# Kernel optimization log

Hardware: AMD Instinct MI355X
Metric: run time of the kernel (lower is better)

## Reference

```python
import jax, jax.numpy as jnp
import numpy as np

H = 512; W = 512; PH = 16; PW = 16; Q = 3; JITTER = 1e-06
NH = H // PH; NW = W // PW; P = NH * NW
B = 64


def setup_inputs() -> dict:
    key = jax.random.key(0)
    k0, k1, k2, k3, k4 = jax.random.split(key, 5)
    x = jax.random.normal(k0, (B, H, W), dtype=jnp.float32)
    logits = jax.random.normal(k1, (P, Q), dtype=jnp.float32)
    mu = jax.random.normal(k2, (P, Q, 2), dtype=jnp.float32) * 0.3
    sigma = jnp.exp(jax.random.normal(k3, (P, Q, 2), dtype=jnp.float32) * 0.3)
    bias = jax.random.normal(k4, (P, PH, PW), dtype=jnp.float32)
    return {"x": x, "logits": logits, "mu": mu, "sigma": sigma, "bias": bias}


def _make_S(logits, mu, sigma):
    # logits: (P,Q), mu/sigma: (P,Q,2) -> S: (P,PH,PW)
    w = jax.nn.softmax(logits, axis=-1)            # (P,Q)
    fy = jnp.fft.fftfreq(PH).astype(jnp.float32)   # (PH,)
    fx = jnp.fft.fftfreq(PW).astype(jnp.float32)   # (PW,)
    mu_y = mu[..., 0][:, :, None, None]            # (P,Q,1,1)
    mu_x = mu[..., 1][:, :, None, None]
    sg_y = sigma[..., 0][:, :, None, None]
    sg_x = sigma[..., 1][:, :, None, None]
    fy_b = fy[None, None, :, None]                 # (1,1,PH,1)
    fx_b = fx[None, None, None, :]                 # (1,1,1,PW)
    g1 = jnp.exp(-0.5 * (((fy_b - mu_y) / sg_y) ** 2 + ((fx_b - mu_x) / sg_x) ** 2))
    g2 = jnp.exp(-0.5 * (((fy_b + mu_y) / sg_y) ** 2 + ((fx_b + mu_x) / sg_x) ** 2))
    # weighted sum over mixture components Q
    S = jnp.einsum('pq,pqhw->phw', w, g1 + g2) + JITTER
    return S


def reference(x, logits, mu, sigma, bias):
    # x: (B,H,W) -> (B,H,W)
    S = _make_S(logits, mu, sigma)                                  # (P,PH,PW)
    x_p = x.reshape(B, NH, PH, NW, PW)
    x_p = x_p.transpose(1, 3, 0, 2, 4).reshape(P, B, PH, PW)        # (P,B,PH,PW)
    Xf = jnp.fft.fftn(x_p, axes=(-2, -1))                           # complex64
    y_p = jnp.fft.ifftn(Xf * S[:, None, :, :], axes=(-2, -1)).real  # (P,B,PH,PW)
    y_p = y_p + bias[:, None, :, :]
    y = y_p.reshape(NH, NW, B, PH, PW)
    y = y.transpose(2, 0, 3, 1, 4).reshape(B, H, W)
    return y
```

## Files before the change

kernel.cpp:

```cpp
#include <hip/hip_runtime.h>
#include <math.h>

#define HH 512
#define WW 512
#define PHH 16
#define PWW 16
#define QQ 3
#define NHH 32
#define NWW 32
#define PP 1024
#define BB 64

__device__ __constant__ float TWC[8] = {
    1.0f,  0.92387953251f,  0.70710678119f,  0.38268343236f,
    0.0f, -0.38268343236f, -0.70710678119f, -0.92387953251f};
__device__ __constant__ float TWS[8] = {
    0.0f, -0.38268343236f, -0.70710678119f, -0.92387953251f,
   -1.0f, -0.92387953251f, -0.70710678119f, -0.38268343236f};

template <int SGN>
__device__ __forceinline__ void fft16(float* re, float* im) {
#define SWAP_(a, b)                              \
  { float t = re[a]; re[a] = re[b]; re[b] = t;   \
    t = im[a]; im[a] = im[b]; im[b] = t; }
  SWAP_(1, 8) SWAP_(2, 4) SWAP_(3, 12) SWAP_(5, 10) SWAP_(7, 14) SWAP_(11, 13)
#undef SWAP_
#pragma unroll
  for (int len = 2; len <= 16; len <<= 1) {
    const int half = len >> 1;
    const int tstep = 16 / len;
#pragma unroll
    for (int i = 0; i < 16; i += len) {
#pragma unroll
      for (int j = 0; j < half; ++j) {
        const float wr = TWC[j * tstep];
        const float wi = (SGN > 0) ? TWS[j * tstep] : -TWS[j * tstep];
        const int a = i + j;
        const int c = i + j + half;
        const float tr = re[c] * wr - im[c] * wi;
        const float ti = re[c] * wi + im[c] * wr;
        re[c] = re[a] - tr;
        im[c] = im[a] - ti;
        re[a] = re[a] + tr;
        im[a] = im[a] + ti;
      }
    }
  }
}

__global__ __launch_bounds__(256) void psm_kernel(
    const float* __restrict__ x, const float* __restrict__ logits,
    const float* __restrict__ mu, const float* __restrict__ sigma,
    const float* __restrict__ bias, float* __restrict__ out) {
  __shared__ float S_lds[256];
  __shared__ float t_re[16 * 272];
  __shared__ float t_im[16 * 272];

  const int tid = threadIdx.x;
  const int p = blockIdx.x >> 2;
  const int b0 = (blockIdx.x & 3) << 4;
  const int g = tid >> 4;
  const int r = tid & 15;
  const int b = b0 + g;
  const int nh = p >> 5;
  const int nw = p & 31;

  {
    const int fy_i = tid >> 4;
    const int fx_i = tid & 15;
    const float fy = (float)(fy_i < 8 ? fy_i : fy_i - 16) * (1.0f / 16.0f);
    const float fx = (float)(fx_i < 8 ? fx_i : fx_i - 16) * (1.0f / 16.0f);
    const float l0 = logits[p * QQ + 0];
    const float l1 = logits[p * QQ + 1];
    const float l2 = logits[p * QQ + 2];
    const float lm = fmaxf(l0, fmaxf(l1, l2));
    const float e0 = __expf(l0 - lm);
    const float e1 = __expf(l1 - lm);
    const float e2 = __expf(l2 - lm);
    const float inv = 1.0f / (e0 + e1 + e2);
    const float wq[3] = {e0 * inv, e1 * inv, e2 * inv};
    float s = 0.0f;
#pragma unroll
    for (int q = 0; q < QQ; ++q) {
      const float muy = mu[(p * QQ + q) * 2 + 0];
      const float mux = mu[(p * QQ + q) * 2 + 1];
      const float isy = 1.0f / sigma[(p * QQ + q) * 2 + 0];
      const float isx = 1.0f / sigma[(p * QQ + q) * 2 + 1];
      const float dy1 = (fy - muy) * isy;
      const float dx1 = (fx - mux) * isx;
      const float dy2 = (fy + muy) * isy;
      const float dx2 = (fx + mux) * isx;
      const float g1 = __expf(-0.5f * (dy1 * dy1 + dx1 * dx1));
      const float g2 = __expf(-0.5f * (dy2 * dy2 + dx2 * dx2));
      s += wq[q] * (g1 + g2);
    }
    S_lds[tid] = (s + 1e-6f) * (1.0f / 256.0f);
  }
  __syncthreads();

  const size_t rowoff =
      (size_t)b * (HH * WW) + (size_t)(nh * PHH + r) * WW + (size_t)(nw * PWW);
  const float* xrow = x + rowoff;
  float re[16], im[16];
#pragma unroll
  for (int c4 = 0; c4 < 4; ++c4) {
    const float4 v = ((const float4*)xrow)[c4];
    re[c4 * 4 + 0] = v.x;
    re[c4 * 4 + 1] = v.y;
    re[c4 * 4 + 2] = v.z;
    re[c4 * 4 + 3] = v.w;
  }
#pragma unroll
  for (int c = 0; c < 16; ++c) im[c] = 0.0f;

  fft16<1>(re, im);

  float* mre = &t_re[g * 272];
  float* mim = &t_im[g * 272];
#pragma unroll
  for (int c = 0; c < 16; ++c) {
    mre[r * 17 + c] = re[c];
    mim[r * 17 + c] = im[c];
  }
  __syncthreads();
#pragma unroll
  for (int k = 0; k < 16; ++k) {
    re[k] = mre[k * 17 + r];
    im[k] = mim[k * 17 + r];
  }
  __syncthreads();

  fft16<1>(re, im);
#pragma unroll
  for (int k = 0; k < 16; ++k) {
    const float s = S_lds[k * 16 + r];
    re[k] *= s;
    im[k] *= s;
  }
  fft16<-1>(re, im);

#pragma unroll
  for (int k = 0; k < 16; ++k) {
    mre[k * 17 + r] = re[k];
    mim[k * 17 + r] = im[k];
  }
  __syncthreads();
#pragma unroll
  for (int c = 0; c < 16; ++c) {
    re[c] = mre[r * 17 + c];
    im[c] = mim[r * 17 + c];
  }

  fft16<-1>(re, im);

  const float* brow = bias + (size_t)p * 256 + (size_t)r * 16;
  float* orow = out + rowoff;
#pragma unroll
  for (int c4 = 0; c4 < 4; ++c4) {
    const float4 bv = ((const float4*)brow)[c4];
    float4 o;
    o.x = re[c4 * 4 + 0] + bv.x;
    o.y = re[c4 * 4 + 1] + bv.y;
    o.z = re[c4 * 4 + 2] + bv.z;
    o.w = re[c4 * 4 + 3] + bv.w;
    ((float4*)orow)[c4] = o;
  }
}

extern "C" void kernel_launch(void* const* d_in, const int* in_sizes, int n_in,
                              void* d_out, int out_size, void* d_ws,
                              size_t ws_size, hipStream_t stream) {
  (void)in_sizes;
  (void)n_in;
  (void)out_size;
  (void)d_ws;
  (void)ws_size;
  const float* x = (const float*)d_in[0];
  const float* logits = (const float*)d_in[1];
  const float* mu = (const float*)d_in[2];
  const float* sigma = (const float*)d_in[3];
  const float* bias = (const float*)d_in[4];
  float* out = (float*)d_out;

  psm_kernel<<<dim3(PP * 4), dim3(256), 0, stream>>>(x, logits, mu, sigma,
                                                     bias, out);
}
```

Before: 148.0 us.

## Replace LDS transposes with wavefront shuffle transposes and prefetch input rows

```diff
diff --git a/kernel.cpp b/kernel.cpp
--- a/kernel.cpp
+++ b/kernel.cpp
@@ -48,13 +48,35 @@
   }
 }
 
+__device__ __forceinline__ void transpose16(float* re, float* im, int r) {
+#pragma unroll
+  for (int s = 1; s <= 8; s <<= 1) {
+    const bool hi = (r & s) != 0;
+#pragma unroll
+    for (int j0 = 0; j0 < 16; ++j0) {
+      if ((j0 & s) == 0) {
+        const int j1 = j0 | s;
+        float sr = hi ? re[j0] : re[j1];
+        float si = hi ? im[j0] : im[j1];
+        sr = __shfl_xor(sr, s, 64);
+        si = __shfl_xor(si, s, 64);
+        if (hi) {
+          re[j0] = sr;
+          im[j0] = si;
+        } else {
+          re[j1] = sr;
+          im[j1] = si;
+        }
+      }
+    }
+  }
+}
+
 __global__ __launch_bounds__(256) void psm_kernel(
     const float* __restrict__ x, const float* __restrict__ logits,
     const float* __restrict__ mu, const float* __restrict__ sigma,
     const float* __restrict__ bias, float* __restrict__ out) {
   __shared__ float S_lds[256];
-  __shared__ float t_re[16 * 272];
-  __shared__ float t_im[16 * 272];
 
   const int tid = threadIdx.x;
   const int p = blockIdx.x >> 2;
@@ -64,6 +86,14 @@
   const int b = b0 + g;
   const int nh = p >> 5;
   const int nw = p & 31;
+
+  const size_t rowoff =
+      (size_t)b * (HH * WW) + (size_t)(nh * PHH + r) * WW + (size_t)(nw * PWW);
+  const float* xrow = x + rowoff;
+  float4 xv0 = ((const float4*)xrow)[0];
+  float4 xv1 = ((const float4*)xrow)[1];
+  float4 xv2 = ((const float4*)xrow)[2];
+  float4 xv3 = ((const float4*)xrow)[3];
 
   {
     const int fy_i = tid >> 4;
@@ -98,38 +128,16 @@
   }
   __syncthreads();
 
-  const size_t rowoff =
-      (size_t)b * (HH * WW) + (size_t)(nh * PHH + r) * WW + (size_t)(nw * PWW);
-  const float* xrow = x + rowoff;
   float re[16], im[16];
-#pragma unroll
-  for (int c4 = 0; c4 < 4; ++c4) {
-    const float4 v = ((const float4*)xrow)[c4];
-    re[c4 * 4 + 0] = v.x;
-    re[c4 * 4 + 1] = v.y;
-    re[c4 * 4 + 2] = v.z;
-    re[c4 * 4 + 3] = v.w;
-  }
+  re[0] = xv0.x;  re[1] = xv0.y;  re[2] = xv0.z;  re[3] = xv0.w;
+  re[4] = xv1.x;  re[5] = xv1.y;  re[6] = xv1.z;  re[7] = xv1.w;
+  re[8] = xv2.x;  re[9] = xv2.y;  re[10] = xv2.z; re[11] = xv2.w;
+  re[12] = xv3.x; re[13] = xv3.y; re[14] = xv3.z; re[15] = xv3.w;
 #pragma unroll
   for (int c = 0; c < 16; ++c) im[c] = 0.0f;
-
   fft16<1>(re, im);
 
-  float* mre = &t_re[g * 272];
-  float* mim = &t_im[g * 272];
-#pragma unroll
-  for (int c = 0; c < 16; ++c) {
-    mre[r * 17 + c] = re[c];
-    mim[r * 17 + c] = im[c];
-  }
-  __syncthreads();
-#pragma unroll
-  for (int k = 0; k < 16; ++k) {
-    re[k] = mre[k * 17 + r];
-    im[k] = mim[k * 17 + r];
-  }
-  __syncthreads();
-
+  transpose16(re, im, r);
   fft16<1>(re, im);
 #pragma unroll
   for (int k = 0; k < 16; ++k) {
@@ -139,18 +147,7 @@
   }
   fft16<-1>(re, im);
 
-#pragma unroll
-  for (int k = 0; k < 16; ++k) {
-    mre[k * 17 + r] = re[k];
-    mim[k * 17 + r] = im[k];
-  }
-  __syncthreads();
-#pragma unroll
-  for (int c = 0; c < 16; ++c) {
-    re[c] = mre[r * 17 + c];
-    im[c] = mim[r * 17 + c];
-  }
-
+  transpose16(re, im, r);
   fft16<-1>(re, im);
 
   const float* brow = bias + (size_t)p * 256 + (size_t)r * 16;
```

Measured after the change: 314.0 us. 2.12x slower.

## Pack two real images into one complex FFT per thread

Applied to the files above, without the earlier changes.

```diff
diff --git a/kernel.cpp b/kernel.cpp
--- a/kernel.cpp
+++ b/kernel.cpp
@@ -57,13 +57,26 @@
   __shared__ float t_im[16 * 272];
 
   const int tid = threadIdx.x;
-  const int p = blockIdx.x >> 2;
-  const int b0 = (blockIdx.x & 3) << 4;
+  const int p = blockIdx.x >> 1;
+  const int b0 = (blockIdx.x & 1) << 5;
   const int g = tid >> 4;
   const int r = tid & 15;
-  const int b = b0 + g;
+  const int b1 = b0 + 2 * g;
   const int nh = p >> 5;
   const int nw = p & 31;
+
+  const size_t rowbase =
+      (size_t)(nh * PHH + r) * WW + (size_t)(nw * PWW);
+  const float* x1 = x + (size_t)b1 * (HH * WW) + rowbase;
+  const float* x2 = x1 + (size_t)(HH * WW);
+  const float4 a0 = ((const float4*)x1)[0];
+  const float4 a1 = ((const float4*)x1)[1];
+  const float4 a2 = ((const float4*)x1)[2];
+  const float4 a3 = ((const float4*)x1)[3];
+  const float4 c0 = ((const float4*)x2)[0];
+  const float4 c1 = ((const float4*)x2)[1];
+  const float4 c2 = ((const float4*)x2)[2];
+  const float4 c3 = ((const float4*)x2)[3];
 
   {
     const int fy_i = tid >> 4;
@@ -96,23 +109,16 @@
     }
     S_lds[tid] = (s + 1e-6f) * (1.0f / 256.0f);
   }
-  __syncthreads();
 
-  const size_t rowoff =
-      (size_t)b * (HH * WW) + (size_t)(nh * PHH + r) * WW + (size_t)(nw * PWW);
-  const float* xrow = x + rowoff;
   float re[16], im[16];
-#pragma unroll
-  for (int c4 = 0; c4 < 4; ++c4) {
-    const float4 v = ((const float4*)xrow)[c4];
-    re[c4 * 4 + 0] = v.x;
-    re[c4 * 4 + 1] = v.y;
-    re[c4 * 4 + 2] = v.z;
-    re[c4 * 4 + 3] = v.w;
-  }
-#pragma unroll
-  for (int c = 0; c < 16; ++c) im[c] = 0.0f;
-
+  re[0] = a0.x;  re[1] = a0.y;  re[2] = a0.z;  re[3] = a0.w;
+  re[4] = a1.x;  re[5] = a1.y;  re[6] = a1.z;  re[7] = a1.w;
+  re[8] = a2.x;  re[9] = a2.y;  re[10] = a2.z; re[11] = a2.w;
+  re[12] = a3.x; re[13] = a3.y; re[14] = a3.z; re[15] = a3.w;
+  im[0] = c0.x;  im[1] = c0.y;  im[2] = c0.z;  im[3] = c0.w;
+  im[4] = c1.x;  im[5] = c1.y;  im[6] = c1.z;  im[7] = c1.w;
+  im[8] = c2.x;  im[9] = c2.y;  im[10] = c2.z; im[11] = c2.w;
+  im[12] = c3.x; im[13] = c3.y; im[14] = c3.z; im[15] = c3.w;
   fft16<1>(re, im);
 
   float* mre = &t_re[g * 272];
@@ -128,7 +134,6 @@
     re[k] = mre[k * 17 + r];
     im[k] = mim[k * 17 + r];
   }
-  __syncthreads();
 
   fft16<1>(re, im);
 #pragma unroll
@@ -139,6 +144,7 @@
   }
   fft16<-1>(re, im);
 
+  __syncthreads();
 #pragma unroll
   for (int k = 0; k < 16; ++k) {
     mre[k * 17 + r] = re[k];
@@ -154,16 +160,22 @@
   fft16<-1>(re, im);
 
   const float* brow = bias + (size_t)p * 256 + (size_t)r * 16;
-  float* orow = out + rowoff;
+  float* o1 = out + (size_t)b1 * (HH * WW) + rowbase;
+  float* o2 = o1 + (size_t)(HH * WW);
 #pragma unroll
   for (int c4 = 0; c4 < 4; ++c4) {
     const float4 bv = ((const float4*)brow)[c4];
-    float4 o;
-    o.x = re[c4 * 4 + 0] + bv.x;
-    o.y = re[c4 * 4 + 1] + bv.y;
-    o.z = re[c4 * 4 + 2] + bv.z;
-    o.w = re[c4 * 4 + 3] + bv.w;
-    ((float4*)orow)[c4] = o;
+    float4 u, v;
+    u.x = re[c4 * 4 + 0] + bv.x;
+    u.y = re[c4 * 4 + 1] + bv.y;
+    u.z = re[c4 * 4 + 2] + bv.z;
+    u.w = re[c4 * 4 + 3] + bv.w;
+    v.x = im[c4 * 4 + 0] + bv.x;
+    v.y = im[c4 * 4 + 1] + bv.y;
+    v.z = im[c4 * 4 + 2] + bv.z;
+    v.w = im[c4 * 4 + 3] + bv.w;
+    ((float4*)o1)[c4] = u;
+    ((float4*)o2)[c4] = v;
   }
 }
 
@@ -182,6 +194,6 @@
   const float* bias = (const float*)d_in[4];
   float* out = (float*)d_out;
 
-  psm_kernel<<<dim3(PP * 4), dim3(256), 0, stream>>>(x, logits, mu, sigma,
+  psm_kernel<<<dim3(PP * 2), dim3(256), 0, stream>>>(x, logits, mu, sigma,
                                                      bias, out);
 }
```

Result: slower. 151.9 us (+2.6%).
